# Performance work log

Hardware: AMD Instinct MI355X
Metric: run time of the kernel (lower is better)

The kernel has to match this reference:

```python
import math
import jax, jax.numpy as jnp
import numpy as np

V, D, DEPTH, H, DH, FF = 32000, 1024, 4, 16, 64, 4096
B, N = 1, 2048


def setup_inputs() -> dict:
    key = jax.random.key(0)
    ks = jax.random.split(key, 8)
    s = 0.02
    return {
        "x": jax.random.randint(ks[0], (B, N), 0, V, dtype=jnp.int32),
        "token_emb": jax.random.normal(ks[1], (V, D), jnp.float32) * s,
        "attn_gamma": jnp.ones((DEPTH, D), jnp.float32),
        "w_qkv": jax.random.normal(ks[2], (DEPTH, D, 3 * H * DH), jnp.float32) * s,
        "w_attn_out": jax.random.normal(ks[3], (DEPTH, H * DH, D), jnp.float32) * s,
        "ff_gamma": jnp.ones((DEPTH, D), jnp.float32),
        "w_ff1": jax.random.normal(ks[4], (DEPTH, D, FF), jnp.float32) * s,
        "b_ff1": jnp.zeros((DEPTH, FF), jnp.float32),
        "w_ff2": jax.random.normal(ks[5], (DEPTH, FF, D), jnp.float32) * s,
        "b_ff2": jnp.zeros((DEPTH, D), jnp.float32),
        "final_gamma": jnp.ones((D,), jnp.float32),
        "w_logits": jax.random.normal(ks[6], (D, V), jnp.float32) * s,
    }


def rms_norm(x, gamma):
    # F.normalize(x, dim=-1) * sqrt(D) * gamma
    norm = jnp.sqrt(jnp.sum(x * x, axis=-1, keepdims=True))
    return x / jnp.maximum(norm, 1e-12) * (x.shape[-1] ** 0.5) * gamma


def rope_cos_sin(n, dh, dtype):
    # lucidrains rotary-embedding-torch default: interleaved pairs
    inv_freq = 1.0 / (10000.0 ** (jnp.arange(0, dh, 2, dtype=jnp.float32) / dh))
    freqs = jnp.arange(n, dtype=jnp.float32)[:, None] * inv_freq[None, :]  # [n, dh/2]
    freqs = jnp.repeat(freqs, 2, axis=-1)  # [n, dh]
    return jnp.cos(freqs).astype(dtype), jnp.sin(freqs).astype(dtype)


def rotate_half(x):
    x1 = x[..., 0::2]
    x2 = x[..., 1::2]
    return jnp.stack((-x2, x1), axis=-1).reshape(x.shape)


def apply_rope(t, cos, sin):
    # t: [b, h, n, dh]; cos/sin: [n, dh]
    return t * cos[None, None] + rotate_half(t) * sin[None, None]


def decoder_forward(x, token_emb, attn_gamma, w_qkv, w_attn_out, ff_gamma,
                    w_ff1, b_ff1, w_ff2, b_ff2, final_gamma, w_logits):
    b, n = x.shape
    h = token_emb[x]  # [b, n, D]
    cos, sin = rope_cos_sin(n, DH, h.dtype)
    causal = jnp.triu(jnp.ones((n, n), bool), k=1)
    scale = DH ** -0.5
    neg = -jnp.finfo(h.dtype).max
    for l in range(DEPTH):
        # attention block
        xn = rms_norm(h, attn_gamma[l])
        qkv = xn @ w_qkv[l]  # [b, n, 3*H*DH]
        qkv = qkv.reshape(b, n, 3, H, DH).transpose(2, 0, 3, 1, 4)  # [3, b, H, n, DH]
        q, k, v = qkv[0], qkv[1], qkv[2]
        q = apply_rope(q, cos, sin)
        k = apply_rope(k, cos, sin)
        sim = jnp.einsum('bhid,bhjd->bhij', q, k) * scale
        sim = jnp.where(causal, neg, sim)
        attn = jax.nn.softmax(sim, axis=-1)
        out = jnp.einsum('bhij,bhjd->bhid', attn, v)
        out = out.transpose(0, 2, 1, 3).reshape(b, n, H * DH) @ w_attn_out[l]
        h = h + out
        # feedforward block
        fn = rms_norm(h, ff_gamma[l])
        ff = jax.nn.gelu(fn @ w_ff1[l] + b_ff1[l], approximate=False) @ w_ff2[l] + b_ff2[l]
        h = h + ff
    return rms_norm(h, final_gamma) @ w_logits


def reference(x, token_emb, attn_gamma, w_qkv, w_attn_out, ff_gamma,
              w_ff1, b_ff1, w_ff2, b_ff2, final_gamma, w_logits):
    return decoder_forward(x, token_emb, attn_gamma, w_qkv, w_attn_out, ff_gamma,
                           w_ff1, b_ff1, w_ff2, b_ff2, final_gamma, w_logits)
```

## Files before the change

### kernel.cpp

```cpp
#include <hip/hip_runtime.h>
#include <math.h>


#define NSEQ 2048
#define DMODEL 1024
#define NH 16
#define DHEAD 64
#define FFD 4096
#define VOC 32000
#define NLAYER 4

typedef unsigned short u16;
typedef short bf16x8 __attribute__((ext_vector_type(8)));
typedef float f32x4 __attribute__((ext_vector_type(4)));

__device__ __forceinline__ u16 f2bf(float f) {
  unsigned int u = __builtin_bit_cast(unsigned int, f);
  u += 0x7fffu + ((u >> 16) & 1u);
  return (u16)(u >> 16);
}

__device__ __forceinline__ void gload16(const void* g, void* l) {
  __builtin_amdgcn_global_load_lds((__attribute__((address_space(1))) void*)g,
                                   (__attribute__((address_space(3))) void*)l,
                                   16, 0, 0);
}

__device__ __forceinline__ f32x4 mfma16x32(bf16x8 a, bf16x8 b, f32x4 c) {
  return __builtin_amdgcn_mfma_f32_16x16x32_bf16(a, b, c, 0, 0, 0);
}

template <int N>
__device__ __forceinline__ void waitvm() {
  if constexpr (N == 0) asm volatile("s_waitcnt vmcnt(0)" ::: "memory");
  else if constexpr (N == 3) asm volatile("s_waitcnt vmcnt(3)" ::: "memory");
  else if constexpr (N == 4) asm volatile("s_waitcnt vmcnt(4)" ::: "memory");
  else if constexpr (N == 6) asm volatile("s_waitcnt vmcnt(6)" ::: "memory");
  else if constexpr (N == 8) asm volatile("s_waitcnt vmcnt(8)" ::: "memory");
}


__global__ __launch_bounds__(256) void k_embed(const int* __restrict__ x,
                                               const float* __restrict__ emb,
                                               float* __restrict__ h) {
  const int n = blockIdx.x, t = threadIdx.x;
  const int tok = x[n];
  reinterpret_cast<float4*>(h + (size_t)n * DMODEL)[t] =
      reinterpret_cast<const float4*>(emb + (size_t)tok * DMODEL)[t];
}

__global__ void k_rope(float* __restrict__ ct, float* __restrict__ st) {
  const int n = blockIdx.x, p = threadIdx.x;
  const double inv = exp(-(double)(2 * p) / 64.0 * log(10000.0));
  const double a = (double)n * inv;
  ct[n * 32 + p] = (float)cos(a);
  st[n * 32 + p] = (float)sin(a);
}

__global__ __launch_bounds__(256) void k_transpose(const float* __restrict__ in0,
                                                   u16* __restrict__ out0,
                                                   int K, int Nc,
                                                   size_t ls_in, size_t ls_out) {
  const float* in = in0 + blockIdx.z * ls_in;
  u16* out = out0 + blockIdx.z * ls_out;
  __shared__ float tile[64][65];
  const int kb = blockIdx.x * 64, nb = blockIdx.y * 64;
  const int tr = threadIdx.x >> 4;
  const int tc = threadIdx.x & 15;
#pragma unroll
  for (int r = 0; r < 64; r += 16) {
    const float4 v = *reinterpret_cast<const float4*>(
        &in[(size_t)(kb + r + tr) * Nc + nb + tc * 4]);
    tile[r + tr][tc * 4 + 0] = v.x;
    tile[r + tr][tc * 4 + 1] = v.y;
    tile[r + tr][tc * 4 + 2] = v.z;
    tile[r + tr][tc * 4 + 3] = v.w;
  }
  __syncthreads();
#pragma unroll
  for (int r = 0; r < 64; r += 16) {
    const int n = r + tr;
    ushort4 o;
    o.x = f2bf(tile[tc * 4 + 0][n]);
    o.y = f2bf(tile[tc * 4 + 1][n]);
    o.z = f2bf(tile[tc * 4 + 2][n]);
    o.w = f2bf(tile[tc * 4 + 3][n]);
    *reinterpret_cast<ushort4*>(&out[(size_t)(nb + n) * K + kb + tc * 4]) = o;
  }
}

__global__ __launch_bounds__(256) void k_rmsnorm(const float* __restrict__ h,
                                                 const float* __restrict__ gamma,
                                                 u16* __restrict__ out) {
  __shared__ float red[4];
  const int n = blockIdx.x, t = threadIdx.x;
  const float4 v = reinterpret_cast<const float4*>(h + (size_t)n * DMODEL)[t];
  float ss = v.x * v.x + v.y * v.y + v.z * v.z + v.w * v.w;
#pragma unroll
  for (int off = 32; off; off >>= 1) ss += __shfl_down(ss, off);
  if ((t & 63) == 0) red[t >> 6] = ss;
  __syncthreads();
  const float tot = red[0] + red[1] + red[2] + red[3];
  const float inv = 32.0f / fmaxf(sqrtf(tot), 1e-12f);
  const float4 g = reinterpret_cast<const float4*>(gamma)[t];
  ushort4 o;
  o.x = f2bf(v.x * inv * g.x);
  o.y = f2bf(v.y * inv * g.y);
  o.z = f2bf(v.z * inv * g.z);
  o.w = f2bf(v.w * inv * g.w);
  reinterpret_cast<ushort4*>(out + (size_t)n * DMODEL)[t] = o;
}

#define EPI_STORE 0
#define EPI_ADD 1
#define EPI_GELU 2
#define EPI_BIAS_ADD 3
#define EPI_QKV 4

__device__ __forceinline__ bf16x8 ldsfragT(const char* base, int row, int lg) {
  return *reinterpret_cast<const bf16x8*>(
      base + row * 64 + (((lg ^ (row & 3) ^ ((row >> 2) & 3)) & 3) << 4));
}

template <int EPI, int BM>
__global__ __launch_bounds__(256) void k_gemmT(
    const u16* __restrict__ A, const u16* __restrict__ BT, int K, int Nc,
    int NMB, const float* __restrict__ bias, const float* __restrict__ add,
    float* __restrict__ outf, u16* __restrict__ outb,
    u16* __restrict__ Qr, u16* __restrict__ Kr, u16* __restrict__ VT,
    const float* __restrict__ ct, const float* __restrict__ st) {
  constexpr int MFR = BM / 32;
  constexpr int ABYTES = BM * 64;
  constexpr int BUFB = ABYTES + 8192;
  constexpr int SL = (BM == 128) ? 4 : 3;
  __shared__ alignas(16) char sm[4 * BUFB];
  const int nt = K >> 5;
  const int nwg = gridDim.x;
  int swz = blockIdx.x;
  if ((nwg & 7) == 0) swz = (swz & 7) * (nwg >> 3) + (swz >> 3);
  const int mb = swz % NMB, nb = swz / NMB;
  const int m0 = mb * BM, n0 = nb * 128;

  const int tid = threadIdx.x, w = tid >> 6, lane = tid & 63;
  const int wr = w >> 1, wc = w & 1;
  const int lr = lane & 15, lg = lane >> 4;

  const int srow = tid >> 2;
  const int gslot = (tid & 3) ^ (srow & 3) ^ ((srow >> 2) & 3);
  const u16* ga0 = A + (size_t)(m0 + srow) * K + gslot * 8;
  const u16* ga1 = A + (size_t)(m0 + (BM == 128 ? 64 : 0) + srow) * K + gslot * 8;
  const u16* gb0 = BT + (size_t)(n0 + srow) * K + gslot * 8;
  const u16* gb1 = BT + (size_t)(n0 + 64 + srow) * K + gslot * 8;
  const int ldOff = tid * 16;

  auto stage = [&](int b) {
    char* base = sm + b * BUFB;
    gload16(ga0, base + ldOff);
    if constexpr (BM == 128) gload16(ga1, base + 4096 + ldOff);
    gload16(gb0, base + ABYTES + ldOff);
    gload16(gb1, base + ABYTES + 4096 + ldOff);
    ga0 += 32; gb0 += 32; gb1 += 32;
    if constexpr (BM == 128) ga1 += 32;
  };

  stage(0);
  stage(1);
  stage(2);
  waitvm<2 * SL>();
  __builtin_amdgcn_s_barrier();

  f32x4 acc[MFR][4] = {};
  int cur = 0;
  for (int t = 0; t < nt; ++t) {
    const char* Ab = sm + cur * BUFB;
    const char* Bb = Ab + ABYTES;
    bf16x8 af[MFR], bf[4];
#pragma unroll
    for (int i = 0; i < MFR; ++i)
      af[i] = ldsfragT(Ab, wr * (BM / 2) + i * 16 + lr, lg);
#pragma unroll
    for (int i = 0; i < 4; ++i)
      bf[i] = ldsfragT(Bb, wc * 64 + i * 16 + lr, lg);
    if (t + 3 < nt) stage((cur + 3) & 3);
    __builtin_amdgcn_s_setprio(1);
#pragma unroll
    for (int mi = 0; mi < MFR; ++mi)
#pragma unroll
      for (int nj = 0; nj < 4; ++nj)
        acc[mi][nj] = mfma16x32(af[mi], bf[nj], acc[mi][nj]);
    __builtin_amdgcn_s_setprio(0);
    if (t + 1 < nt) {
      __builtin_amdgcn_sched_barrier(0);
      if (t + 3 < nt)      waitvm<2 * SL>();
      else if (t + 2 < nt) waitvm<SL>();
      else                 waitvm<0>();
      __builtin_amdgcn_s_barrier();
      __builtin_amdgcn_sched_barrier(0);
    }
    cur = (cur + 1) & 3;
  }

  if constexpr (EPI == EPI_QKV) {
    const int which = n0 >> 10;
    const int hh = ((n0 & 1023) >> 6) + wc;
#pragma unroll
    for (int mi = 0; mi < MFR; ++mi) {
#pragma unroll
      for (int nj = 0; nj < 4; ++nj) {
        const int d = nj * 16 + lr;
#pragma unroll
        for (int r = 0; r < 4; ++r) {
          const int row = m0 + wr * (BM / 2) + mi * 16 + lg * 4 + r;
          const float v = acc[mi][nj][r];
          if (which == 2) {
            VT[((size_t)hh * DHEAD + d) * NSEQ + row] = f2bf(v);
          } else {
            const float part = __shfl_xor(v, 1);
            const float sgn = (d & 1) ? 1.0f : -1.0f;
            const float c = ct[row * 32 + (d >> 1)];
            const float s_ = st[row * 32 + (d >> 1)];
            const u16 o = f2bf(v * c + sgn * part * s_);
            u16* dst = (which == 0) ? Qr : Kr;
            dst[((size_t)hh * NSEQ + row) * DHEAD + d] = o;
          }
        }
      }
    }
    return;
  }
#pragma unroll
  for (int mi = 0; mi < MFR; ++mi) {
#pragma unroll
    for (int nj = 0; nj < 4; ++nj) {
      const int col = n0 + wc * 64 + nj * 16 + lr;
#pragma unroll
      for (int r = 0; r < 4; ++r) {
        const int row = m0 + wr * (BM / 2) + mi * 16 + lg * 4 + r;
        const size_t idx = (size_t)row * Nc + col;
        float v = acc[mi][nj][r];
        if (EPI == EPI_GELU) {
          v += bias[col];
          v = 0.5f * v * (1.0f + erff(v * 0.70710678118654752f));
          outb[idx] = f2bf(v);
        } else if (EPI == EPI_ADD) {
          outf[idx] = v + add[idx];
        } else if (EPI == EPI_BIAS_ADD) {
          outf[idx] = v + bias[col] + add[idx];
        } else {
          outf[idx] = v;
        }
      }
    }
  }
}

template <int EPI>
__global__ __launch_bounds__(256, 2) void k_gemmW(
    const u16* __restrict__ A, const u16* __restrict__ BT, int K, int Nc,
    const float* __restrict__ bias, float* __restrict__ outf,
    u16* __restrict__ outb) {
  constexpr int ABYTES = 8192;
  constexpr int BUFB = ABYTES + 16384;
  __shared__ alignas(16) char sm[3 * BUFB];
  const int nt = K >> 5;
  const int NMB = 16;
  const int nwg = gridDim.x;
  int swz = blockIdx.x;
  if ((nwg & 7) == 0) swz = (swz & 7) * (nwg >> 3) + (swz >> 3);
  const int mb = swz % NMB, nb = swz / NMB;
  const int m0 = mb * 128, n0 = nb * 256;

  const int tid = threadIdx.x, w = tid >> 6, lane = tid & 63;
  const int wr = w >> 1, wc = w & 1;
  const int lr = lane & 15, lg = lane >> 4;

  const int srow = tid >> 2;
  const int gslot = (tid & 3) ^ (srow & 3) ^ ((srow >> 2) & 3);
  const u16* ga0 = A + (size_t)(m0 + srow) * K + gslot * 8;
  const u16* ga1 = A + (size_t)(m0 + 64 + srow) * K + gslot * 8;
  const u16* gb0 = BT + (size_t)(n0 + srow) * K + gslot * 8;
  const u16* gb1 = BT + (size_t)(n0 + 64 + srow) * K + gslot * 8;
  const u16* gb2 = BT + (size_t)(n0 + 128 + srow) * K + gslot * 8;
  const u16* gb3 = BT + (size_t)(n0 + 192 + srow) * K + gslot * 8;
  const int ldOff = tid * 16;

  auto stage = [&](int b) {
    char* base = sm + b * BUFB;
    gload16(ga0, base + ldOff);
    gload16(ga1, base + 4096 + ldOff);
    gload16(gb0, base + ABYTES + ldOff);
    gload16(gb1, base + ABYTES + 4096 + ldOff);
    gload16(gb2, base + ABYTES + 8192 + ldOff);
    gload16(gb3, base + ABYTES + 12288 + ldOff);
    ga0 += 32; ga1 += 32; gb0 += 32; gb1 += 32; gb2 += 32; gb3 += 32;
  };

  stage(0);
  stage(1);
  waitvm<6>();
  __builtin_amdgcn_s_barrier();

  f32x4 acc[4][8] = {};
  int cur = 0, nx2 = 2;
  for (int t = 0; t < nt; ++t) {
    const char* Ab = sm + cur * BUFB;
    const char* Bb = Ab + ABYTES;
    const bool pf = (t + 2 < nt);
    bf16x8 af[4], bf[8];
#pragma unroll
    for (int i = 0; i < 4; ++i)
      af[i] = ldsfragT(Ab, wr * 64 + i * 16 + lr, lg);
#pragma unroll
    for (int i = 0; i < 8; ++i)
      bf[i] = ldsfragT(Bb, wc * 128 + i * 16 + lr, lg);
    if (pf) stage(nx2);
    __builtin_amdgcn_s_setprio(1);
#pragma unroll
    for (int mi = 0; mi < 4; ++mi)
#pragma unroll
      for (int nj = 0; nj < 8; ++nj)
        acc[mi][nj] = mfma16x32(af[mi], bf[nj], acc[mi][nj]);
    __builtin_amdgcn_s_setprio(0);
    if (t + 1 < nt) {
      __builtin_amdgcn_sched_barrier(0);
      if (pf) waitvm<6>();
      else    waitvm<0>();
      __builtin_amdgcn_s_barrier();
      __builtin_amdgcn_sched_barrier(0);
    }
    cur = (cur == 2) ? 0 : cur + 1;
    nx2 = (nx2 == 2) ? 0 : nx2 + 1;
  }

#pragma unroll
  for (int mi = 0; mi < 4; ++mi) {
#pragma unroll
    for (int nj = 0; nj < 8; ++nj) {
      const int col = n0 + wc * 128 + nj * 16 + lr;
#pragma unroll
      for (int r = 0; r < 4; ++r) {
        const int row = m0 + wr * 64 + mi * 16 + lg * 4 + r;
        const size_t idx = (size_t)row * Nc + col;
        float v = acc[mi][nj][r];
        if (EPI == EPI_GELU) {
          v += bias[col];
          v = 0.5f * v * (1.0f + erff(v * 0.70710678118654752f));
          outb[idx] = f2bf(v);
        } else {
          outf[idx] = v;
        }
      }
    }
  }
}

__global__ __launch_bounds__(256) void k_attn(const u16* __restrict__ Qr,
                                              const u16* __restrict__ Kr,
                                              const u16* __restrict__ VT,
                                              u16* __restrict__ O) {
  __shared__ alignas(16) u16 Pl[4][16 * 32];
  const int hh = blockIdx.y;
  const int w = threadIdx.x >> 6, lane = threadIdx.x & 63;
  const int lr = lane & 15, lg = lane >> 4;
  const int q0 = blockIdx.x * 64 + w * 16;
  const u16* Qh = Qr + (size_t)hh * NSEQ * DHEAD;
  const u16* Kh = Kr + (size_t)hh * NSEQ * DHEAD;
  const u16* Vh = VT + (size_t)hh * DHEAD * NSEQ;
  u16* Pw = Pl[w];

  const bf16x8 aq0 = *reinterpret_cast<const bf16x8*>(Qh + (q0 + lr) * DHEAD + lg * 8);
  const bf16x8 aq1 = *reinterpret_cast<const bf16x8*>(Qh + (q0 + lr) * DHEAD + 32 + lg * 8);

  f32x4 o0 = {}, o1 = {}, o2 = {}, o3 = {};
  float m[4], l[4];
#pragma unroll
  for (int r = 0; r < 4; ++r) { m[r] = -1e30f; l[r] = 0.0f; }

  const int jend = q0 + 15;

  auto loadK = [&](int j0, bf16x8* bk) {
    bk[0] = *reinterpret_cast<const bf16x8*>(Kh + (j0 + lr) * DHEAD + lg * 8);
    bk[1] = *reinterpret_cast<const bf16x8*>(Kh + (j0 + lr) * DHEAD + 32 + lg * 8);
    bk[2] = *reinterpret_cast<const bf16x8*>(Kh + (j0 + 16 + lr) * DHEAD + lg * 8);
    bk[3] = *reinterpret_cast<const bf16x8*>(Kh + (j0 + 16 + lr) * DHEAD + 32 + lg * 8);
  };
  auto loadV = [&](int j0, bf16x8* vv) {
    const u16* vb = Vh + j0 + lg * 8;
    vv[0] = *reinterpret_cast<const bf16x8*>(vb + (0 + lr) * NSEQ);
    vv[1] = *reinterpret_cast<const bf16x8*>(vb + (16 + lr) * NSEQ);
    vv[2] = *reinterpret_cast<const bf16x8*>(vb + (32 + lr) * NSEQ);
    vv[3] = *reinterpret_cast<const bf16x8*>(vb + (48 + lr) * NSEQ);
  };

  bf16x8 bk[4], vv[4], bkN[4], vvN[4];
  loadK(0, bk);
  loadV(0, vv);

  for (int j0 = 0; j0 <= jend; j0 += 32) {
    if (j0 + 32 <= jend) { loadK(j0 + 32, bkN); loadV(j0 + 32, vvN); }

    f32x4 s0 = {}, s1 = {};
    s0 = mfma16x32(aq0, bk[0], s0);
    s0 = mfma16x32(aq1, bk[1], s0);
    s1 = mfma16x32(aq0, bk[2], s1);
    s1 = mfma16x32(aq1, bk[3], s1);

    float sv0[4], sv1[4], pm[4];
#pragma unroll
    for (int r = 0; r < 4; ++r) {
      const int irow = q0 + lg * 4 + r;
      sv0[r] = (j0 + lr > irow) ? -1e30f : s0[r] * 0.125f;
      sv1[r] = (j0 + 16 + lr > irow) ? -1e30f : s1[r] * 0.125f;
      pm[r] = fmaxf(sv0[r], sv1[r]);
    }
#pragma unroll
    for (int off = 1; off < 16; off <<= 1)
#pragma unroll
      for (int r = 0; r < 4; ++r) pm[r] = fmaxf(pm[r], __shfl_xor(pm[r], off));
    float p0[4], p1[4], rs[4];
    f32x4 fv;
#pragma unroll
    for (int r = 0; r < 4; ++r) {
      const float mn = fmaxf(m[r], pm[r]);
      fv[r] = __expf(m[r] - mn);
      m[r] = mn;
      p0[r] = __expf(sv0[r] - mn);
      p1[r] = __expf(sv1[r] - mn);
      rs[r] = p0[r] + p1[r];
    }
#pragma unroll
    for (int off = 1; off < 16; off <<= 1)
#pragma unroll
      for (int r = 0; r < 4; ++r) rs[r] += __shfl_xor(rs[r], off);
#pragma unroll
    for (int r = 0; r < 4; ++r) l[r] = l[r] * fv[r] + rs[r];
    o0 *= fv; o1 *= fv; o2 *= fv; o3 *= fv;

#pragma unroll
    for (int r = 0; r < 4; ++r) {
      Pw[(lg * 4 + r) * 32 + lr] = f2bf(p0[r]);
      Pw[(lg * 4 + r) * 32 + 16 + lr] = f2bf(p1[r]);
    }
    const bf16x8 pa = *reinterpret_cast<const bf16x8*>(Pw + lr * 32 + lg * 8);
    o0 = mfma16x32(pa, vv[0], o0);
    o1 = mfma16x32(pa, vv[1], o1);
    o2 = mfma16x32(pa, vv[2], o2);
    o3 = mfma16x32(pa, vv[3], o3);

#pragma unroll
    for (int i = 0; i < 4; ++i) { bk[i] = bkN[i]; vv[i] = vvN[i]; }
  }

#pragma unroll
  for (int r = 0; r < 4; ++r) {
    const int row = q0 + lg * 4 + r;
    const float invl = 1.0f / l[r];
    u16* orow = O + (size_t)row * DMODEL + hh * DHEAD;
    orow[0 * 16 + lr] = f2bf(o0[r] * invl);
    orow[1 * 16 + lr] = f2bf(o1[r] * invl);
    orow[2 * 16 + lr] = f2bf(o2[r] * invl);
    orow[3 * 16 + lr] = f2bf(o3[r] * invl);
  }
}


extern "C" void kernel_launch(void* const* d_in, const int* in_sizes, int n_in,
                              void* d_out, int out_size, void* d_ws, size_t ws_size,
                              hipStream_t stream) {
  (void)in_sizes; (void)n_in;
  const int* x = (const int*)d_in[0];
  const float* emb = (const float*)d_in[1];
  const float* attn_gamma = (const float*)d_in[2];
  const float* w_qkv = (const float*)d_in[3];
  const float* w_attn_out = (const float*)d_in[4];
  const float* ff_gamma = (const float*)d_in[5];
  const float* w_ff1 = (const float*)d_in[6];
  const float* b_ff1 = (const float*)d_in[7];
  const float* w_ff2 = (const float*)d_in[8];
  const float* b_ff2 = (const float*)d_in[9];
  const float* final_gamma = (const float*)d_in[10];
  const float* w_logits = (const float*)d_in[11];
  float* out = (float*)d_out;

  const size_t EARLY_NEED = 176ull << 20;
  const size_t FINAL_NEED = 72ull << 20;
  char* earlyBase;
  char* finalBase;
  if (ws_size >= EARLY_NEED + FINAL_NEED) {
    earlyBase = (char*)d_ws;
    finalBase = (char*)d_ws + EARLY_NEED;
  } else if (ws_size >= FINAL_NEED && (size_t)out_size * 4 >= EARLY_NEED) {
    earlyBase = (char*)d_out;
    finalBase = (char*)d_ws;
  } else {
    return;
  }
  size_t eoff = 0, foff = 0;
  auto ealloc = [&](size_t b) { void* p = earlyBase + eoff; eoff += (b + 255) & ~(size_t)255; return p; };
  auto falloc = [&](size_t b) { void* p = finalBase + foff; foff += (b + 255) & ~(size_t)255; return p; };

  u16* wqkvT = (u16*)ealloc((size_t)NLAYER * 3072 * DMODEL * 2);
  u16* wattnT = (u16*)ealloc((size_t)NLAYER * DMODEL * DMODEL * 2);
  u16* wff1T = (u16*)ealloc((size_t)NLAYER * FFD * DMODEL * 2);
  u16* wff2T = (u16*)ealloc((size_t)NLAYER * DMODEL * FFD * 2);
  float* h = (float*)ealloc((size_t)NSEQ * DMODEL * 4);
  u16* Qr = (u16*)ealloc((size_t)NH * NSEQ * DHEAD * 2);
  u16* Kr = (u16*)ealloc((size_t)NH * NSEQ * DHEAD * 2);
  u16* VTb = (u16*)ealloc((size_t)NH * NSEQ * DHEAD * 2);
  u16* Ob = (u16*)ealloc((size_t)NSEQ * DMODEL * 2);
  u16* ff1b = (u16*)ealloc((size_t)NSEQ * FFD * 2);
  float* ct = (float*)ealloc((size_t)NSEQ * 32 * 4);
  float* st = (float*)ealloc((size_t)NSEQ * 32 * 4);
  u16* wlogT = (u16*)falloc((size_t)VOC * DMODEL * 2);
  u16* xn = (u16*)falloc((size_t)NSEQ * DMODEL * 2);

  k_rope<<<dim3(NSEQ), dim3(32), 0, stream>>>(ct, st);
  k_transpose<<<dim3(16, 48, NLAYER), 256, 0, stream>>>(
      w_qkv, wqkvT, DMODEL, 3072, (size_t)DMODEL * 3072, (size_t)3072 * DMODEL);
  k_transpose<<<dim3(16, 16, NLAYER), 256, 0, stream>>>(
      w_attn_out, wattnT, DMODEL, DMODEL, (size_t)DMODEL * DMODEL, (size_t)DMODEL * DMODEL);
  k_transpose<<<dim3(16, 64, NLAYER), 256, 0, stream>>>(
      w_ff1, wff1T, DMODEL, FFD, (size_t)DMODEL * FFD, (size_t)FFD * DMODEL);
  k_transpose<<<dim3(64, 16, NLAYER), 256, 0, stream>>>(
      w_ff2, wff2T, FFD, DMODEL, (size_t)FFD * DMODEL, (size_t)DMODEL * FFD);
  k_transpose<<<dim3(16, 500, 1), 256, 0, stream>>>(
      w_logits, wlogT, DMODEL, VOC, 0, 0);

  k_embed<<<dim3(NSEQ), 256, 0, stream>>>(x, emb, h);

  for (int lyr = 0; lyr < NLAYER; ++lyr) {
    k_rmsnorm<<<dim3(NSEQ), 256, 0, stream>>>(h, attn_gamma + (size_t)lyr * DMODEL, xn);
    k_gemmT<EPI_QKV, 64><<<dim3(32 * 24), 256, 0, stream>>>(
        xn, wqkvT + (size_t)lyr * 3072 * DMODEL, DMODEL, 3072, 32,
        nullptr, nullptr, nullptr, nullptr, Qr, Kr, VTb, ct, st);
    k_attn<<<dim3(NSEQ / 64, NH), 256, 0, stream>>>(Qr, Kr, VTb, Ob);
    k_gemmT<EPI_ADD, 64><<<dim3(32 * 8), 256, 0, stream>>>(
        Ob, wattnT + (size_t)lyr * DMODEL * DMODEL, DMODEL, DMODEL, 32,
        nullptr, h, h, nullptr, nullptr, nullptr, nullptr, nullptr, nullptr);
    k_rmsnorm<<<dim3(NSEQ), 256, 0, stream>>>(h, ff_gamma + (size_t)lyr * DMODEL, xn);
    k_gemmT<EPI_GELU, 128><<<dim3(16 * 32), 256, 0, stream>>>(
        xn, wff1T + (size_t)lyr * FFD * DMODEL, DMODEL, FFD, 16,
        b_ff1 + (size_t)lyr * FFD, nullptr, nullptr, ff1b,
        nullptr, nullptr, nullptr, nullptr, nullptr);
    k_gemmT<EPI_BIAS_ADD, 64><<<dim3(32 * 8), 256, 0, stream>>>(
        ff1b, wff2T + (size_t)lyr * DMODEL * FFD, FFD, DMODEL, 32,
        b_ff2 + (size_t)lyr * DMODEL, h, h, nullptr,
        nullptr, nullptr, nullptr, nullptr, nullptr);
  }

  k_rmsnorm<<<dim3(NSEQ), 256, 0, stream>>>(h, final_gamma, xn);
  k_gemmW<EPI_STORE><<<dim3(16 * 125), 256, 0, stream>>>(
      xn, wlogT, DMODEL, VOC, nullptr, out, nullptr);
}
```

Before: 1.278 ms.

## Parametrize GEMM tile width and reorder attention blocks for causal load balance

The GEMM kernel gains a BN template parameter, so the N=1024 projections (attn-out, ff2) use 64x64 tiles and launch 512 workgroups instead of 256. FF1 moves from 128x128 to 64x128 tiles, also doubling its grid. Attention becomes a 1D grid where the second half of the heads walks query blocks in reverse, so that long and short causal blocks interleave across the GPU. Smaller tiles raise per-FLOP load traffic and lower MFMA reuse in exchange for better CU occupancy.

Measured after the change: 1.205 ms. 1.06x faster.

```diff
diff --git a/kernel.cpp b/kernel.cpp
--- a/kernel.cpp
+++ b/kernel.cpp
@@ -33,6 +33,7 @@
 template <int N>
 __device__ __forceinline__ void waitvm() {
   if constexpr (N == 0) asm volatile("s_waitcnt vmcnt(0)" ::: "memory");
+  else if constexpr (N == 2) asm volatile("s_waitcnt vmcnt(2)" ::: "memory");
   else if constexpr (N == 3) asm volatile("s_waitcnt vmcnt(3)" ::: "memory");
   else if constexpr (N == 4) asm volatile("s_waitcnt vmcnt(4)" ::: "memory");
   else if constexpr (N == 6) asm volatile("s_waitcnt vmcnt(6)" ::: "memory");
@@ -122,7 +123,7 @@
       base + row * 64 + (((lg ^ (row & 3) ^ ((row >> 2) & 3)) & 3) << 4));
 }
 
-template <int EPI, int BM>
+template <int EPI, int BM, int BN>
 __global__ __launch_bounds__(256) void k_gemmT(
     const u16* __restrict__ A, const u16* __restrict__ BT, int K, int Nc,
     int NMB, const float* __restrict__ bias, const float* __restrict__ add,
@@ -130,16 +131,18 @@
     u16* __restrict__ Qr, u16* __restrict__ Kr, u16* __restrict__ VT,
     const float* __restrict__ ct, const float* __restrict__ st) {
   constexpr int MFR = BM / 32;
+  constexpr int NFR = BN / 32;
   constexpr int ABYTES = BM * 64;
-  constexpr int BUFB = ABYTES + 8192;
-  constexpr int SL = (BM == 128) ? 4 : 3;
+  constexpr int BBYTES = BN * 64;
+  constexpr int BUFB = ABYTES + BBYTES;
+  constexpr int SL = BM / 64 + BN / 64;
   __shared__ alignas(16) char sm[4 * BUFB];
   const int nt = K >> 5;
   const int nwg = gridDim.x;
   int swz = blockIdx.x;
   if ((nwg & 7) == 0) swz = (swz & 7) * (nwg >> 3) + (swz >> 3);
   const int mb = swz % NMB, nb = swz / NMB;
-  const int m0 = mb * BM, n0 = nb * 128;
+  const int m0 = mb * BM, n0 = nb * BN;
 
   const int tid = threadIdx.x, w = tid >> 6, lane = tid & 63;
   const int wr = w >> 1, wc = w & 1;
@@ -150,7 +153,7 @@
   const u16* ga0 = A + (size_t)(m0 + srow) * K + gslot * 8;
   const u16* ga1 = A + (size_t)(m0 + (BM == 128 ? 64 : 0) + srow) * K + gslot * 8;
   const u16* gb0 = BT + (size_t)(n0 + srow) * K + gslot * 8;
-  const u16* gb1 = BT + (size_t)(n0 + 64 + srow) * K + gslot * 8;
+  const u16* gb1 = BT + (size_t)(n0 + (BN == 128 ? 64 : 0) + srow) * K + gslot * 8;
   const int ldOff = tid * 16;
 
   auto stage = [&](int b) {
@@ -158,9 +161,10 @@
     gload16(ga0, base + ldOff);
     if constexpr (BM == 128) gload16(ga1, base + 4096 + ldOff);
     gload16(gb0, base + ABYTES + ldOff);
-    gload16(gb1, base + ABYTES + 4096 + ldOff);
-    ga0 += 32; gb0 += 32; gb1 += 32;
+    if constexpr (BN == 128) gload16(gb1, base + ABYTES + 4096 + ldOff);
+    ga0 += 32; gb0 += 32;
     if constexpr (BM == 128) ga1 += 32;
+    if constexpr (BN == 128) gb1 += 32;
   };
 
   stage(0);
@@ -169,24 +173,24 @@
   waitvm<2 * SL>();
   __builtin_amdgcn_s_barrier();
 
-  f32x4 acc[MFR][4] = {};
+  f32x4 acc[MFR][NFR] = {};
   int cur = 0;
   for (int t = 0; t < nt; ++t) {
     const char* Ab = sm + cur * BUFB;
     const char* Bb = Ab + ABYTES;
-    bf16x8 af[MFR], bf[4];
+    bf16x8 af[MFR], bf[NFR];
 #pragma unroll
     for (int i = 0; i < MFR; ++i)
       af[i] = ldsfragT(Ab, wr * (BM / 2) + i * 16 + lr, lg);
 #pragma unroll
-    for (int i = 0; i < 4; ++i)
-      bf[i] = ldsfragT(Bb, wc * 64 + i * 16 + lr, lg);
+    for (int i = 0; i < NFR; ++i)
+      bf[i] = ldsfragT(Bb, wc * (BN / 2) + i * 16 + lr, lg);
     if (t + 3 < nt) stage((cur + 3) & 3);
     __builtin_amdgcn_s_setprio(1);
 #pragma unroll
     for (int mi = 0; mi < MFR; ++mi)
 #pragma unroll
-      for (int nj = 0; nj < 4; ++nj)
+      for (int nj = 0; nj < NFR; ++nj)
         acc[mi][nj] = mfma16x32(af[mi], bf[nj], acc[mi][nj]);
     __builtin_amdgcn_s_setprio(0);
     if (t + 1 < nt) {
@@ -206,7 +210,7 @@
 #pragma unroll
     for (int mi = 0; mi < MFR; ++mi) {
 #pragma unroll
-      for (int nj = 0; nj < 4; ++nj) {
+      for (int nj = 0; nj < NFR; ++nj) {
         const int d = nj * 16 + lr;
 #pragma unroll
         for (int r = 0; r < 4; ++r) {
@@ -231,8 +235,8 @@
 #pragma unroll
   for (int mi = 0; mi < MFR; ++mi) {
 #pragma unroll
-    for (int nj = 0; nj < 4; ++nj) {
-      const int col = n0 + wc * 64 + nj * 16 + lr;
+    for (int nj = 0; nj < NFR; ++nj) {
+      const int col = n0 + wc * (BN / 2) + nj * 16 + lr;
 #pragma unroll
       for (int r = 0; r < 4; ++r) {
         const int row = m0 + wr * (BM / 2) + mi * 16 + lg * 4 + r;
@@ -359,10 +363,13 @@
                                               const u16* __restrict__ VT,
                                               u16* __restrict__ O) {
   __shared__ alignas(16) u16 Pl[4][16 * 32];
-  const int hh = blockIdx.y;
+  const int id = blockIdx.x;
+  int qb, hh;
+  if (id < 256) { qb = id & 31; hh = id >> 5; }
+  else          { qb = 31 - (id & 31); hh = 8 + ((id - 256) >> 5); }
   const int w = threadIdx.x >> 6, lane = threadIdx.x & 63;
   const int lr = lane & 15, lg = lane >> 4;
-  const int q0 = blockIdx.x * 64 + w * 16;
+  const int q0 = qb * 64 + w * 16;
   const u16* Qh = Qr + (size_t)hh * NSEQ * DHEAD;
   const u16* Kh = Kr + (size_t)hh * NSEQ * DHEAD;
   const u16* Vh = VT + (size_t)hh * DHEAD * NSEQ;
@@ -530,19 +537,19 @@
 
   for (int lyr = 0; lyr < NLAYER; ++lyr) {
     k_rmsnorm<<<dim3(NSEQ), 256, 0, stream>>>(h, attn_gamma + (size_t)lyr * DMODEL, xn);
-    k_gemmT<EPI_QKV, 64><<<dim3(32 * 24), 256, 0, stream>>>(
+    k_gemmT<EPI_QKV, 64, 128><<<dim3(32 * 24), 256, 0, stream>>>(
         xn, wqkvT + (size_t)lyr * 3072 * DMODEL, DMODEL, 3072, 32,
         nullptr, nullptr, nullptr, nullptr, Qr, Kr, VTb, ct, st);
-    k_attn<<<dim3(NSEQ / 64, NH), 256, 0, stream>>>(Qr, Kr, VTb, Ob);
-    k_gemmT<EPI_ADD, 64><<<dim3(32 * 8), 256, 0, stream>>>(
+    k_attn<<<dim3(512), 256, 0, stream>>>(Qr, Kr, VTb, Ob);
+    k_gemmT<EPI_ADD, 64, 64><<<dim3(32 * 16), 256, 0, stream>>>(
         Ob, wattnT + (size_t)lyr * DMODEL * DMODEL, DMODEL, DMODEL, 32,
         nullptr, h, h, nullptr, nullptr, nullptr, nullptr, nullptr, nullptr);
     k_rmsnorm<<<dim3(NSEQ), 256, 0, stream>>>(h, ff_gamma + (size_t)lyr * DMODEL, xn);
-    k_gemmT<EPI_GELU, 128><<<dim3(16 * 32), 256, 0, stream>>>(
-        xn, wff1T + (size_t)lyr * FFD * DMODEL, DMODEL, FFD, 16,
+    k_gemmT<EPI_GELU, 64, 128><<<dim3(32 * 32), 256, 0, stream>>>(
+        xn, wff1T + (size_t)lyr * FFD * DMODEL, DMODEL, FFD, 32,
         b_ff1 + (size_t)lyr * FFD, nullptr, nullptr, ff1b,
         nullptr, nullptr, nullptr, nullptr, nullptr);
-    k_gemmT<EPI_BIAS_ADD, 64><<<dim3(32 * 8), 256, 0, stream>>>(
+    k_gemmT<EPI_BIAS_ADD, 64, 64><<<dim3(32 * 16), 256, 0, stream>>>(
         ff1b, wff2T + (size_t)lyr * DMODEL * FFD, FFD, DMODEL, 32,
         b_ff2 + (size_t)lyr * DMODEL, h, h, nullptr,
         nullptr, nullptr, nullptr, nullptr, nullptr);
```
